# Kernel optimization log

Measured on AMD Instinct MI355X. Metric: run time of the kernel, lower is better.

The kernel has to match this reference:

```python
import jax, jax.numpy as jnp
import numpy as np

D_MODEL = 2048
D_STATE = 64
D_CONV = 4
EXPAND = 2
HEADDIM = 64
NGROUPS = 1
CHUNK = 64
D_INNER = D_MODEL * EXPAND          # 4096
NHEADS = D_INNER // HEADDIM         # 64
D_IN_PROJ = 2 * D_INNER + 2 * NGROUPS * D_STATE + NHEADS
BATCH, SEQLEN = 2, 4096
RMS_EPS = 1e-6


def elu_plus_one(x):
    return jax.nn.elu(x) + 1.0


def softplus(x):
    return jnp.where(x > 20, x, jnp.log1p(jnp.exp(x)))


def causal_conv1d(x, w, b):
    # x: (B, L, D), w: (K, D) depthwise kernel, b: (D,)
    Bsz, L, Dn = x.shape
    k = w.shape[0]
    xp = jnp.transpose(jnp.pad(x, ((0, 0), (k - 1, 0), (0, 0))), (0, 2, 1))  # (B, D, L+K-1)
    kern = jnp.transpose(w, (1, 0))[:, None, :]  # (D, 1, K)
    y = jax.lax.conv_general_dilated(xp, kern, (1,), 'VALID',
                                     feature_group_count=Dn,
                                     dimension_numbers=('NCH', 'OIH', 'NCH'))
    return jnp.transpose(y, (0, 2, 1)) + b


def ssd_chunked(q, k, v, a, chunk_size):
    # SSD / chunked linear attention with per-step scalar decay.
    # Recurrence: h_t = a_t * h_{t-1} + k_t v_t^T ; y_t = q_t @ h_t
    # q,k: (B,H,L,N); v: (B,H,L,P); a: (B,H,L) in (0,1)
    Bsz, H, L, N = q.shape
    S = chunk_size
    C = L // S
    qc = q.reshape(Bsz, H, C, S, N)
    kc = k.reshape(Bsz, H, C, S, N)
    vc = v.reshape(Bsz, H, C, S, -1)
    la = jnp.log(a).reshape(Bsz, H, C, S)
    cs = jnp.cumsum(la, axis=-1)                 # inclusive cumsum of log-decay within chunk
    causal = jnp.tril(jnp.ones((S, S), bool))
    # decay from position j to i (j<=i): exp(cs_i - cs_j)
    logdec = jnp.where(causal, cs[..., :, None] - cs[..., None, :], -jnp.inf)
    att = jnp.einsum('bhcsn,bhctn->bhcst', qc, kc) * jnp.exp(logdec)
    y_intra = jnp.einsum('bhcst,bhctp->bhcsp', att, vc)
    total = cs[..., -1]                           # (B,H,C) total log-decay per chunk
    k_scaled = kc * jnp.exp(total[..., None, None] - cs[..., None])
    states = jnp.einsum('bhcsn,bhcsp->bhcnp', k_scaled, vc)  # per-chunk state update
    d_t = jnp.moveaxis(jnp.exp(total), 2, 0)      # (C,B,H)
    s_t = jnp.moveaxis(states, 2, 0)              # (C,B,H,N,P)

    def step(h, inp):
        d, s = inp
        return d[..., None, None] * h + s, h      # emit state at chunk start

    _, h_prev = jax.lax.scan(step, jnp.zeros_like(s_t[0]), (d_t, s_t))
    h_prev = jnp.moveaxis(h_prev, 0, 2)           # (B,H,C,N,P)
    y_inter = jnp.einsum('bhcsn,bhcnp->bhcsp', qc * jnp.exp(cs)[..., None], h_prev)
    return (y_intra + y_inter).reshape(Bsz, H, L, -1)


def setup_inputs() -> dict:
    key = jax.random.key(0)
    k0, k1, k2, k3 = jax.random.split(key, 4)
    u = jax.random.normal(k0, (BATCH, SEQLEN, D_MODEL), jnp.float32)
    in_proj_w = jax.random.normal(k1, (D_MODEL, D_IN_PROJ), jnp.float32) / np.sqrt(D_MODEL)
    conv_weight = jax.random.normal(k2, (D_CONV, D_INNER), jnp.float32) / np.sqrt(D_CONV)
    conv_bias = jnp.zeros((D_INNER,), jnp.float32)
    A_log = jnp.log(jnp.linspace(1.0, 16.0, NHEADS)).astype(jnp.float32)
    dt_init = jnp.exp(jnp.linspace(np.log(0.001), np.log(0.1), NHEADS))
    dt_bias = (dt_init + jnp.log(-jnp.expm1(-dt_init))).astype(jnp.float32)
    D_param = jnp.ones((NHEADS,), jnp.float32)
    norm_scale = jnp.ones((D_INNER,), jnp.float32)
    out_proj_w = jax.random.normal(k3, (D_INNER, D_MODEL), jnp.float32) / np.sqrt(D_INNER)
    return dict(u=u, in_proj_w=in_proj_w, conv_weight=conv_weight, conv_bias=conv_bias,
                A_log=A_log, dt_bias=dt_bias, D_param=D_param, norm_scale=norm_scale,
                out_proj_w=out_proj_w)


def reference(u, in_proj_w, conv_weight, conv_bias, A_log, dt_bias, D_param, norm_scale, out_proj_w):
    Bsz, L, _ = u.shape
    zxBCdt = u @ in_proj_w
    splits = [D_INNER, 2 * D_INNER, 2 * D_INNER + NGROUPS * D_STATE, 2 * D_INNER + 2 * NGROUPS * D_STATE]
    z, x, B_proj, C_proj, dt_logits = jnp.split(zxBCdt, splits, axis=-1)
    x = jax.nn.silu(causal_conv1d(x, conv_weight, conv_bias))
    B_mat = elu_plus_one(B_proj.reshape(Bsz, L, NGROUPS, D_STATE))
    C_mat = elu_plus_one(C_proj.reshape(Bsz, L, NGROUPS, D_STATE))
    hpg = NHEADS // NGROUPS
    B_mat = jnp.repeat(B_mat, hpg, axis=2)   # (B,L,H,N)
    C_mat = jnp.repeat(C_mat, hpg, axis=2)
    dt = softplus(dt_logits + dt_bias)        # (B,L,H)
    a = jnp.exp(-dt * jnp.exp(A_log))         # (B,L,H), per-step decay
    x_heads = x.reshape(Bsz, L, NHEADS, HEADDIM)
    q = jnp.transpose(C_mat, (0, 2, 1, 3))
    k = jnp.transpose(B_mat, (0, 2, 1, 3))
    v = jnp.transpose(x_heads, (0, 2, 1, 3))
    a_t = jnp.transpose(a, (0, 2, 1))
    y = ssd_chunked(q, k, v, a_t, CHUNK)
    y = y + D_param[None, :, None, None] * v  # skip connection
    y = jnp.transpose(y, (0, 2, 1, 3)).reshape(Bsz, L, D_INNER)
    y = y * jax.lax.rsqrt(jnp.mean(y * y, axis=-1, keepdims=True) + RMS_EPS) * norm_scale
    y = y * jax.nn.silu(z)
    return y @ out_proj_w
```

## Files before the change

kernel.cpp:

```cpp
#include <hip/hip_runtime.h>
#include <hip/hip_bf16.h>
#include <cstdint>
#include <cstddef>

#define BATCH   2
#define SEQLEN  4096
#define DMODEL  2048
#define DINNER  4096
#define NHEADS  64
#define HEADDIM 64
#define DSTATE  64
#define CHUNK   64
#define NCHUNK  (SEQLEN/CHUNK)
#define DPROJ   8384
#define DPROJ_PAD 8448
#define MTOK    (BATCH*SEQLEN)
#define RMS_EPS 1e-6f

typedef __hip_bfloat16 bf16;
typedef __attribute__((ext_vector_type(8))) short bf16x8;
typedef __attribute__((ext_vector_type(4))) float f32x4;

__device__ __forceinline__ float siluf(float x) { return x / (1.f + expf(-x)); }
__device__ __forceinline__ float to_f(float x) { return x; }
__device__ __forceinline__ float to_f(bf16 x) { return __bfloat162float(x); }
__device__ __forceinline__ float bf2f(short s) { bf16 h; *(short*)&h = s; return __bfloat162float(h); }
__device__ __forceinline__ void from_f(float& d, float x) { d = x; }
__device__ __forceinline__ void from_f(bf16& d, float x) { d = __float2bfloat16(x); }

__device__ __forceinline__ void gload16(const void* g, void* l) {
  __builtin_amdgcn_global_load_lds(
      (const __attribute__((address_space(1))) void*)g,
      (__attribute__((address_space(3))) void*)l, 16, 0, 0);
}

template <typename TC, int KT>
__global__ __launch_bounds__(1024, 4) void gemm_w16p2(
    const bf16* __restrict__ A, int lda,
    const bf16* __restrict__ BT, int ldb,
    TC* __restrict__ C, int ldc, int gx) {
  __shared__ __align__(16) bf16 As[4 * 8192];
  __shared__ __align__(16) bf16 Bs[4 * 8192];
  const int tid  = threadIdx.x;
  const int lane = tid & 63;
  const int w    = tid >> 6;
  const int wm   = w >> 2;
  const int wn   = w & 3;
  const int lr   = lane & 15, lg = lane >> 4;
  const int fo   = 8 * (lg ^ ((lr >> 1) & 3));

  int nwg = gridDim.x;
  int bid = (int)blockIdx.x;
  int idx = (bid & 7) * (nwg >> 3) + (bid >> 3);
  int spos = idx % (8 * gx);
  const int m0 = ((idx / (8 * gx)) * 8 + (spos & 7)) * 256;
  const int n0 = (spos >> 3) * 256;

  const int srow = tid >> 2;
  const int ce   = 8 * ((tid & 3) ^ ((tid >> 3) & 3));
  const bf16* pA = A  + (size_t)(m0 + srow) * lda + ce;
  const bf16* pB = BT + (size_t)(n0 + srow) * ldb + ce;
  const int wofs = w * 512;
  const int aRd = (wm * 64 + lr) * 32 + fo;
  const int bRd = (wn * 64 + lr) * 32 + fo;

#define STAGE_A(kt) gload16(pA + ((kt) << 5), As + (((kt) & 3) << 13) + wofs)
#define STAGE_B(kt) gload16(pB + ((kt) << 5), Bs + (((kt) & 3) << 13) + wofs)

  f32x4 acc[4][4];
#pragma unroll
  for (int m = 0; m < 4; ++m)
#pragma unroll
    for (int n = 0; n < 4; ++n) acc[m][n] = (f32x4){0.f, 0.f, 0.f, 0.f};

#define TILE(T) do {                                                         \
    const bf16* Ab = As + (((T) & 3) << 13);                                 \
    const bf16* Bb = Bs + (((T) & 3) << 13);                                 \
    bf16x8 bfv[4], af[4];                                                    \
    _Pragma("unroll")                                                        \
    for (int n = 0; n < 4; ++n) bfv[n] = *(const bf16x8*)&Bb[bRd + n * 512]; \
    _Pragma("unroll")                                                        \
    for (int m = 0; m < 4; ++m) af[m] = *(const bf16x8*)&Ab[aRd + m * 512];  \
    asm volatile("s_waitcnt lgkmcnt(0)" ::: "memory");                       \
    __builtin_amdgcn_sched_barrier(0);                                       \
    __builtin_amdgcn_s_setprio(1);                                           \
    _Pragma("unroll")                                                        \
    for (int m = 0; m < 4; ++m)                                              \
      _Pragma("unroll")                                                      \
      for (int n = 0; n < 4; ++n)                                            \
        acc[m][n] = __builtin_amdgcn_mfma_f32_16x16x32_bf16(af[m], bfv[n], acc[m][n], 0, 0, 0); \
    __builtin_amdgcn_s_setprio(0);                                           \
  } while (0)

#define PERIOD(P, DOSTAGE) do {                                              \
    if (DOSTAGE) { STAGE_A(2 * (P) + 2); STAGE_B(2 * (P) + 2);               \
                   STAGE_A(2 * (P) + 3); STAGE_B(2 * (P) + 3); }             \
    TILE(2 * (P));                                                           \
    TILE(2 * (P) + 1);                                                       \
    asm volatile("s_waitcnt vmcnt(0)" ::: "memory");                         \
    __builtin_amdgcn_s_barrier();                                            \
    __builtin_amdgcn_sched_barrier(0);                                       \
  } while (0)

  STAGE_A(0); STAGE_B(0); STAGE_A(1); STAGE_B(1);
  asm volatile("s_waitcnt vmcnt(0)" ::: "memory");
  __builtin_amdgcn_s_barrier();
  __builtin_amdgcn_sched_barrier(0);

  const int NP = KT / 2;
#pragma unroll 2
  for (int p = 0; p < NP - 1; ++p) PERIOD(p, true);
  PERIOD(NP - 1, false);
#undef PERIOD
#undef TILE
#undef STAGE_A
#undef STAGE_B

  if constexpr (__is_same(TC, bf16)) {
    bf16* Ws = (w < 8 ? As : Bs) + (w & 7) * 4096;
#pragma unroll
    for (int m = 0; m < 4; ++m)
#pragma unroll
      for (int n = 0; n < 4; ++n)
#pragma unroll
        for (int reg = 0; reg < 4; ++reg) {
          int row = m * 16 + lg * 4 + reg;
          int slot = (n * 2 + (lr >> 3)) ^ (row & 7);
          Ws[row * 64 + slot * 8 + (lr & 7)] = __float2bfloat16(acc[m][n][reg]);
        }
    asm volatile("s_waitcnt lgkmcnt(0)" ::: "memory");
#pragma unroll
    for (int i = 0; i < 8; ++i) {
      int row = i * 8 + (lane >> 3);
      bf16x8 v = *(const bf16x8*)&Ws[row * 64 + ((lane & 7) ^ (lane >> 3)) * 8];
      int gcol = n0 + wn * 64 + (lane & 7) * 8;
      *(bf16x8*)&((bf16*)C)[(size_t)(m0 + wm * 64 + row) * ldc + gcol] = v;
    }
  } else {
#pragma unroll
    for (int m = 0; m < 4; ++m)
#pragma unroll
      for (int n = 0; n < 4; ++n) {
        int col = n0 + wn * 64 + n * 16 + lr;
        size_t rbase = (size_t)(m0 + wm * 64 + m * 16 + lg * 4);
#pragma unroll
        for (int reg = 0; reg < 4; ++reg)
          from_f(C[(rbase + reg) * ldc + col], acc[m][n][reg]);
      }
  }
}

template <typename TC, bool MASK>
__global__ __launch_bounds__(256) void gemm_mfma(
    const bf16* __restrict__ A, int lda,
    const bf16* __restrict__ BT, int ldb,
    TC* __restrict__ C, int ldc, int Kdim, int Nvalid) {
  __shared__ __align__(16) bf16 As[128 * 32];
  __shared__ __align__(16) bf16 Bs[128 * 32];
  const int tid  = threadIdx.x;
  const int lane = tid & 63;
  const int w    = tid >> 6;
  const int m0 = blockIdx.y * 128;
  const int n0 = blockIdx.x * 128;

  const int rs0 = w * 32 + (lane >> 2);
  const int ce  = 8 * ((lane & 3) ^ ((lane >> 2) & 3));
  const int fo  = 8 * ((lane >> 4) ^ (lane & 3));
  const int lr  = lane & 15, lg = lane >> 4;
  const int wr = w >> 1, wc = w & 1;

  f32x4 acc[4][4];
#pragma unroll
  for (int m = 0; m < 4; ++m)
#pragma unroll
    for (int n = 0; n < 4; ++n) acc[m][n] = (f32x4){0.f, 0.f, 0.f, 0.f};

  const size_t arow0 = (size_t)(m0 + rs0) * lda;
  const size_t arow1 = (size_t)(m0 + rs0 + 16) * lda;
  const size_t brow0 = (size_t)(n0 + rs0) * ldb;
  const size_t brow1 = (size_t)(n0 + rs0 + 16) * ldb;
  bf16* lA0 = &As[(w * 2 + 0) * 512];
  bf16* lA1 = &As[(w * 2 + 1) * 512];
  bf16* lB0 = &Bs[(w * 2 + 0) * 512];
  bf16* lB1 = &Bs[(w * 2 + 1) * 512];

  for (int k0 = 0; k0 < Kdim; k0 += 32) {
    __syncthreads();
    gload16(A + arow0 + k0 + ce, lA0);
    gload16(A + arow1 + k0 + ce, lA1);
    gload16(BT + brow0 + k0 + ce, lB0);
    gload16(BT + brow1 + k0 + ce, lB1);
    __syncthreads();
    bf16x8 af[4], bfr[4];
#pragma unroll
    for (int m = 0; m < 4; ++m)
      af[m] = *(const bf16x8*)&As[(wr * 64 + m * 16 + lr) * 32 + fo];
#pragma unroll
    for (int n = 0; n < 4; ++n)
      bfr[n] = *(const bf16x8*)&Bs[(wc * 64 + n * 16 + lr) * 32 + fo];
#pragma unroll
    for (int m = 0; m < 4; ++m)
#pragma unroll
      for (int n = 0; n < 4; ++n)
        acc[m][n] = __builtin_amdgcn_mfma_f32_16x16x32_bf16(af[m], bfr[n], acc[m][n], 0, 0, 0);
  }

#pragma unroll
  for (int m = 0; m < 4; ++m)
#pragma unroll
    for (int n = 0; n < 4; ++n) {
      int col = n0 + wc * 64 + n * 16 + lr;
      if (MASK && col >= Nvalid) continue;
      size_t rbase = (size_t)(m0 + wr * 64 + m * 16 + lg * 4);
#pragma unroll
      for (int reg = 0; reg < 4; ++reg)
        from_f(C[(rbase + reg) * ldc + col], acc[m][n][reg]);
    }
}

__global__ __launch_bounds__(256) void cast_bf16_kernel(
    const float* __restrict__ x, bf16* __restrict__ y) {
  size_t i = ((size_t)blockIdx.x * 256 + threadIdx.x) * 4;
  float4 v = *(const float4*)(x + i);
  y[i + 0] = __float2bfloat16(v.x);
  y[i + 1] = __float2bfloat16(v.y);
  y[i + 2] = __float2bfloat16(v.z);
  y[i + 3] = __float2bfloat16(v.w);
}

__global__ __launch_bounds__(256) void transpose_cast_kernel(
    const float* __restrict__ W, bf16* __restrict__ WT, int N, int K) {
  __shared__ float t[32][33];
  int n0 = blockIdx.x * 32, k0 = blockIdx.y * 32;
  int tx = threadIdx.x & 31, ty = threadIdx.x >> 5;
#pragma unroll
  for (int i = 0; i < 4; ++i) {
    int n = n0 + tx;
    t[ty + i * 8][tx] = (n < N) ? W[(size_t)(k0 + ty + i * 8) * N + n] : 0.f;
  }
  __syncthreads();
#pragma unroll
  for (int i = 0; i < 4; ++i) {
    int nn = ty + i * 8;
    WT[(size_t)(n0 + nn) * K + k0 + tx] = __float2bfloat16(t[tx][nn]);
  }
}

__global__ __launch_bounds__(256) void conv_silu_kernel(
    const bf16* __restrict__ zx, const float* __restrict__ cw,
    const float* __restrict__ cb, bf16* __restrict__ xc) {
  int idx = blockIdx.x * 256 + threadIdx.x;
  int d8 = (idx & 511) * 8;
  int g = idx >> 9;
  int m0 = g * 4;
  int l0 = m0 & (SEQLEN - 1);
  int b = m0 >> 12;
  bf16x8 rows[7];
  bf16x8 zvec;
#pragma unroll
  for (int j = 0; j < 8; ++j) zvec[j] = 0;
#pragma unroll
  for (int r = 0; r < 7; ++r) {
    int li = l0 - 3 + r;
    rows[r] = (li >= 0)
        ? *(const bf16x8*)&zx[(size_t)(b * SEQLEN + li) * DPROJ + DINNER + d8]
        : zvec;
  }
  float cwv[4][8], cbv[8];
#pragma unroll
  for (int k = 0; k < 4; ++k) {
    float4 a = *(const float4*)(cw + k * DINNER + d8);
    float4 bb = *(const float4*)(cw + k * DINNER + d8 + 4);
    cwv[k][0] = a.x; cwv[k][1] = a.y; cwv[k][2] = a.z; cwv[k][3] = a.w;
    cwv[k][4] = bb.x; cwv[k][5] = bb.y; cwv[k][6] = bb.z; cwv[k][7] = bb.w;
  }
  {
    float4 a = *(const float4*)(cb + d8);
    float4 bb = *(const float4*)(cb + d8 + 4);
    cbv[0] = a.x; cbv[1] = a.y; cbv[2] = a.z; cbv[3] = a.w;
    cbv[4] = bb.x; cbv[5] = bb.y; cbv[6] = bb.z; cbv[7] = bb.w;
  }
#pragma unroll
  for (int j = 0; j < 4; ++j) {
    float acc[8];
#pragma unroll
    for (int e = 0; e < 8; ++e) acc[e] = cbv[e];
#pragma unroll
    for (int k = 0; k < 4; ++k)
#pragma unroll
      for (int e = 0; e < 8; ++e) acc[e] += bf2f(rows[j + k][e]) * cwv[k][e];
    bf16x8 o;
#pragma unroll
    for (int e = 0; e < 8; ++e) { bf16 h = __float2bfloat16(siluf(acc[e])); o[e] = *(short*)&h; }
    *(bf16x8*)&xc[(size_t)(m0 + j) * DINNER + d8] = o;
  }
}

__global__ __launch_bounds__(256) void prep_cumsum_kernel(
    const bf16* __restrict__ zx, const float* __restrict__ A_log,
    const float* __restrict__ dt_bias, bf16* __restrict__ Bmb,
    bf16* __restrict__ Cmb, float* __restrict__ cs) {
  int bid = blockIdx.x;
  int c = bid & 63, b = bid >> 6;
  int m0 = b * SEQLEN + c * CHUNK;
  int tid = threadIdx.x;
  int s = tid >> 2, grp = (tid & 3) * 16;
  __shared__ float laT[64 * 65];
  __shared__ float segs[4][64];
  const bf16* row = zx + (size_t)(m0 + s) * DPROJ + 2 * DINNER;
  {
    union { bf16x8 v[2]; bf16 hh[16]; } u, o;
    u.v[0] = *(const bf16x8*)&row[grp];
    u.v[1] = *(const bf16x8*)&row[grp + 8];
#pragma unroll
    for (int i = 0; i < 16; ++i) {
      float bv = to_f(u.hh[i]);
      from_f(o.hh[i], bv > 0.f ? bv + 1.f : expf(bv));
    }
    *(bf16x8*)&Bmb[(size_t)(m0 + s) * 64 + grp] = o.v[0];
    *(bf16x8*)&Bmb[(size_t)(m0 + s) * 64 + grp + 8] = o.v[1];
    u.v[0] = *(const bf16x8*)&row[64 + grp];
    u.v[1] = *(const bf16x8*)&row[64 + grp + 8];
#pragma unroll
    for (int i = 0; i < 16; ++i) {
      float cv = to_f(u.hh[i]);
      from_f(o.hh[i], cv > 0.f ? cv + 1.f : expf(cv));
    }
    *(bf16x8*)&Cmb[(size_t)(m0 + s) * 64 + grp] = o.v[0];
    *(bf16x8*)&Cmb[(size_t)(m0 + s) * 64 + grp + 8] = o.v[1];
    u.v[0] = *(const bf16x8*)&row[128 + grp];
    u.v[1] = *(const bf16x8*)&row[128 + grp + 8];
#pragma unroll
    for (int i = 0; i < 16; ++i) {
      int j = grp + i;
      float dtl = to_f(u.hh[i]) + dt_bias[j];
      float dt = dtl > 20.f ? dtl : log1pf(expf(dtl));
      laT[j * 65 + s] = -dt * expf(A_log[j]);
    }
  }
  __syncthreads();
  int j = tid & 63, sg = tid >> 6;
  float p = 0.f;
#pragma unroll
  for (int i = 0; i < 16; ++i) p += laT[j * 65 + sg * 16 + i];
  segs[sg][j] = p;
  __syncthreads();
  float off = (sg > 0 ? segs[0][j] : 0.f) + (sg > 1 ? segs[1][j] : 0.f) +
              (sg > 2 ? segs[2][j] : 0.f);
  float acc = off;
#pragma unroll
  for (int i = 0; i < 16; ++i) {
    acc += laT[j * 65 + sg * 16 + i];
    cs[(size_t)(m0 + sg * 16 + i) * 64 + j] = acc;
  }
}

__global__ __launch_bounds__(256) void states_mfma(
    const bf16* __restrict__ Bmb, const bf16* __restrict__ xc,
    const float* __restrict__ cs, bf16* __restrict__ st) {
  int bid = blockIdx.x;
  int c = bid & 63, h = (bid >> 6) & 63, b = bid >> 12;
  int m0 = b * SEQLEN + c * CHUNK;
  int tid = threadIdx.x, lane = tid & 63, w = tid >> 6;
  int lr = lane & 15, lg = lane >> 4;
  __shared__ bf16 vT[64 * 72];
  __shared__ bf16 kT[64 * 72];
  int s4 = tid >> 2, c16 = (tid & 3) * 16;
  float cstot = cs[(size_t)(m0 + 63) * 64 + h];
  float ws = expf(cstot - cs[(size_t)(m0 + s4) * 64 + h]);
  {
    union { bf16x8 v[2]; bf16 hh[16]; } u;
    const bf16x8* pv = (const bf16x8*)&xc[(size_t)(m0 + s4) * DINNER + h * 64 + c16];
    u.v[0] = pv[0]; u.v[1] = pv[1];
#pragma unroll
    for (int i = 0; i < 16; ++i) vT[(c16 + i) * 72 + s4] = u.hh[i];
    const bf16x8* pk = (const bf16x8*)&Bmb[(size_t)(m0 + s4) * 64 + c16];
    u.v[0] = pk[0]; u.v[1] = pk[1];
#pragma unroll
    for (int i = 0; i < 16; ++i) kT[(c16 + i) * 72 + s4] = __float2bfloat16(to_f(u.hh[i]) * ws);
  }
  __syncthreads();
  f32x4 acc[4];
#pragma unroll
  for (int ct = 0; ct < 4; ++ct) acc[ct] = (f32x4){0.f, 0.f, 0.f, 0.f};
#pragma unroll
  for (int ks = 0; ks < 2; ++ks) {
    bf16x8 af = *(const bf16x8*)&vT[(w * 16 + lr) * 72 + ks * 32 + lg * 8];
#pragma unroll
    for (int ct = 0; ct < 4; ++ct) {
      bf16x8 bf_ = *(const bf16x8*)&kT[(ct * 16 + lr) * 72 + ks * 32 + lg * 8];
      acc[ct] = __builtin_amdgcn_mfma_f32_16x16x32_bf16(af, bf_, acc[ct], 0, 0, 0);
    }
  }
  size_t ob = (((size_t)(b * NHEADS + h)) * NCHUNK + c) * 4096;
#pragma unroll
  for (int ct = 0; ct < 4; ++ct) {
    int n = ct * 16 + lr;
#pragma unroll
    for (int r = 0; r < 4; ++r) {
      int p = w * 16 + lg * 4 + r;
      from_f(st[ob + (size_t)p * 64 + n], acc[ct][r]);
    }
  }
}

__global__ __launch_bounds__(256) void scan_kernel(
    const float* __restrict__ cs, bf16* __restrict__ st) {
  int bid = blockIdx.x;
  int bh = bid >> 2, qq = bid & 3;
  int b = bh >> 6, h = bh & 63;
  int tid = threadIdx.x;
  __shared__ float dec[64];
  if (tid < 64)
    dec[tid] = expf(cs[(size_t)(b * SEQLEN + tid * CHUNK + 63) * 64 + h]);
  int e0 = qq * 1024 + tid * 4;
  float hr[4] = {0.f, 0.f, 0.f, 0.f};
  size_t base = (size_t)bh * NCHUNK * 4096;
  typedef __attribute__((ext_vector_type(4))) short bf16x4;
  union U { bf16x4 v; bf16 hh[4]; };
  U buf[4];
  buf[0].v = *(bf16x4*)(st + base + 0 * 4096 + e0);
  buf[1].v = *(bf16x4*)(st + base + 1 * 4096 + e0);
  buf[2].v = *(bf16x4*)(st + base + 2 * 4096 + e0);
  __syncthreads();
#pragma unroll 4
  for (int c = 0; c < NCHUNK; ++c) {
    if (c + 3 < NCHUNK)
      buf[(c + 3) & 3].v = *(bf16x4*)(st + base + (size_t)(c + 3) * 4096 + e0);
    float d = dec[c];
    U out;
#pragma unroll
    for (int i = 0; i < 4; ++i) {
      float sv = to_f(buf[c & 3].hh[i]);
      from_f(out.hh[i], hr[i]);
      hr[i] = d * hr[i] + sv;
    }
    *(bf16x4*)(st + base + (size_t)c * 4096 + e0) = out.v;
  }
}

__global__ __launch_bounds__(256) void chunk_out_mfma(
    const bf16* __restrict__ Bmb, const bf16* __restrict__ Cmb,
    const bf16* __restrict__ xc, const float* __restrict__ cs,
    const bf16* __restrict__ st, const float* __restrict__ Dp,
    bf16* __restrict__ zx) {
  int bid = blockIdx.x;
  int c = bid & 63, h = (bid >> 6) & 63, b = bid >> 12;
  int m0 = b * SEQLEN + c * CHUNK;
  int tid = threadIdx.x, lane = tid & 63, w = tid >> 6;
  int lr = lane & 15, lg = lane >> 4;
  __shared__ bf16 qL[64 * 72];
  __shared__ bf16 kL[64 * 72];
  __shared__ bf16 A2[64 * 136];
  __shared__ bf16 B2[64 * 136];
  __shared__ float csl[64];
  int s4 = tid >> 2, c16 = (tid & 3) * 16;

  if (tid < 64) csl[tid] = cs[(size_t)(m0 + tid) * 64 + h];
  {
    const bf16x8* pq = (const bf16x8*)&Cmb[(size_t)(m0 + s4) * 64 + c16];
    *(bf16x8*)&qL[s4 * 72 + c16] = pq[0];
    *(bf16x8*)&qL[s4 * 72 + c16 + 8] = pq[1];
    const bf16x8* pk = (const bf16x8*)&Bmb[(size_t)(m0 + s4) * 64 + c16];
    *(bf16x8*)&kL[s4 * 72 + c16] = pk[0];
    *(bf16x8*)&kL[s4 * 72 + c16 + 8] = pk[1];
  }
  {
    union { bf16x8 v[2]; bf16 hh[16]; } u;
    const bf16x8* pv = (const bf16x8*)&xc[(size_t)(m0 + s4) * DINNER + h * 64 + c16];
    u.v[0] = pv[0]; u.v[1] = pv[1];
#pragma unroll
    for (int i = 0; i < 16; ++i) B2[(c16 + i) * 136 + s4] = u.hh[i];
  }
  {
    size_t hb = (((size_t)(b * NHEADS + h)) * NCHUNK + c) * 4096;
    const bf16x8* ph = (const bf16x8*)&st[hb + (size_t)s4 * 64 + c16];
    *(bf16x8*)&B2[s4 * 136 + 64 + c16] = ph[0];
    *(bf16x8*)&B2[s4 * 136 + 64 + c16 + 8] = ph[1];
  }
  __syncthreads();

  f32x4 acc1[4];
#pragma unroll
  for (int ct = 0; ct < 4; ++ct) acc1[ct] = (f32x4){0.f, 0.f, 0.f, 0.f};
#pragma unroll
  for (int ks = 0; ks < 2; ++ks) {
    bf16x8 af = *(const bf16x8*)&qL[(w * 16 + lr) * 72 + ks * 32 + lg * 8];
#pragma unroll
    for (int ct = 0; ct < 4; ++ct) {
      bf16x8 bf_ = *(const bf16x8*)&kL[(ct * 16 + lr) * 72 + ks * 32 + lg * 8];
      acc1[ct] = __builtin_amdgcn_mfma_f32_16x16x32_bf16(af, bf_, acc1[ct], 0, 0, 0);
    }
  }
  {
    float es = expf(csl[s4]);
    union { bf16x8 v[2]; bf16 hh[16]; } u;
    const bf16x8* pq = (const bf16x8*)&qL[s4 * 72 + c16];
    u.v[0] = pq[0]; u.v[1] = pq[1];
#pragma unroll
    for (int i = 0; i < 16; ++i) u.hh[i] = __float2bfloat16(to_f(u.hh[i]) * es);
    *(bf16x8*)&A2[s4 * 136 + 64 + c16] = u.v[0];
    *(bf16x8*)&A2[s4 * 136 + 64 + c16 + 8] = u.v[1];
  }
#pragma unroll
  for (int ct = 0; ct < 4; ++ct) {
    int t = ct * 16 + lr;
#pragma unroll
    for (int r = 0; r < 4; ++r) {
      int s = w * 16 + lg * 4 + r;
      float val = (t <= s) ? acc1[ct][r] * expf(csl[s] - csl[t]) : 0.f;
      A2[s * 136 + t] = __float2bfloat16(val);
    }
  }
  __syncthreads();

  float Dh = Dp[h];
  f32x4 acc2[4];
#pragma unroll
  for (int ct = 0; ct < 4; ++ct) {
    int p = ct * 16 + lr;
#pragma unroll
    for (int r = 0; r < 4; ++r)
      acc2[ct][r] = Dh * to_f(B2[p * 136 + (w * 16 + lg * 4 + r)]);
  }
#pragma unroll
  for (int ks = 0; ks < 4; ++ks) {
    bf16x8 af = *(const bf16x8*)&A2[(w * 16 + lr) * 136 + ks * 32 + lg * 8];
#pragma unroll
    for (int ct = 0; ct < 4; ++ct) {
      bf16x8 bf_ = *(const bf16x8*)&B2[(ct * 16 + lr) * 136 + ks * 32 + lg * 8];
      acc2[ct] = __builtin_amdgcn_mfma_f32_16x16x32_bf16(af, bf_, acc2[ct], 0, 0, 0);
    }
  }
  __syncthreads();
#pragma unroll
  for (int ct = 0; ct < 4; ++ct) {
    int p = ct * 16 + lr;
#pragma unroll
    for (int r = 0; r < 4; ++r)
      qL[(w * 16 + lg * 4 + r) * 72 + p] = __float2bfloat16(acc2[ct][r]);
  }
  __syncthreads();
  {
    const bf16x8* py = (const bf16x8*)&qL[s4 * 72 + c16];
    bf16x8* pg = (bf16x8*)&zx[(size_t)(m0 + s4) * DPROJ + DINNER + h * 64 + c16];
    pg[0] = py[0]; pg[1] = py[1];
  }
}

__global__ __launch_bounds__(256) void rmsnorm_gate_kernel(
    bf16* __restrict__ zx, const float* __restrict__ scale) {
  int m = blockIdx.x;
  int tid = threadIdx.x;
  bf16* row = zx + (size_t)m * DPROJ;
  float vals[16];
  float ss = 0.f;
#pragma unroll
  for (int g = 0; g < 2; ++g) {
    int d8 = (tid + g * 256) * 8;
    bf16x8 yv = *(const bf16x8*)&row[DINNER + d8];
#pragma unroll
    for (int j = 0; j < 8; ++j) {
      float y = bf2f(yv[j]);
      vals[g * 8 + j] = y;
      ss += y * y;
    }
  }
#pragma unroll
  for (int off = 32; off > 0; off >>= 1) ss += __shfl_down(ss, off, 64);
  __shared__ float red[4];
  if ((tid & 63) == 0) red[tid >> 6] = ss;
  __syncthreads();
  float tot = red[0] + red[1] + red[2] + red[3];
  float inv = rsqrtf(tot / (float)DINNER + RMS_EPS);
#pragma unroll
  for (int g = 0; g < 2; ++g) {
    int d8 = (tid + g * 256) * 8;
    bf16x8 zv = *(const bf16x8*)&row[d8];
    const float* sc = scale + d8;
    bf16x8 o;
#pragma unroll
    for (int j = 0; j < 8; ++j) {
      bf16 hh = __float2bfloat16(vals[g * 8 + j] * inv * sc[j] * siluf(bf2f(zv[j])));
      o[j] = *(short*)&hh;
    }
    *(bf16x8*)&row[DINNER + d8] = o;
  }
}

extern "C" void kernel_launch(void* const* d_in, const int* in_sizes, int n_in,
                              void* d_out, int out_size, void* d_ws, size_t ws_size,
                              hipStream_t stream) {
  const float* u       = (const float*)d_in[0];
  const float* Win     = (const float*)d_in[1];
  const float* cw      = (const float*)d_in[2];
  const float* cb      = (const float*)d_in[3];
  const float* A_log   = (const float*)d_in[4];
  const float* dt_bias = (const float*)d_in[5];
  const float* Dp      = (const float*)d_in[6];
  const float* nscale  = (const float*)d_in[7];
  const float* Wout    = (const float*)d_in[8];
  float* out = (float*)d_out;

  bf16* zx = (bf16*)d_ws;
  bf16* xc = zx + (size_t)MTOK * DPROJ;
  bf16* ub = xc;
  bf16* wT = xc + (size_t)MTOK * DINNER;
  bf16* Bmb = wT + (size_t)DPROJ_PAD * DMODEL;
  bf16* Cmb = Bmb + (size_t)MTOK * 64;
  float* cs = (float*)(Cmb + (size_t)MTOK * 64);
  bf16* st = (bf16*)d_out;

  cast_bf16_kernel<<<(MTOK * DMODEL) / (256 * 4), 256, 0, stream>>>(u, ub);
  transpose_cast_kernel<<<dim3(DPROJ_PAD / 32, DMODEL / 32), 256, 0, stream>>>(Win, wT, DPROJ, DMODEL);
  gemm_w16p2<bf16, DMODEL / 32><<<(2 * DINNER / 256) * (MTOK / 256), 1024, 0, stream>>>(
      ub, DMODEL, wT, DMODEL, zx, DPROJ, 2 * DINNER / 256);
  gemm_mfma<bf16, true><<<dim3(2, MTOK / 128), 256, 0, stream>>>(
      ub, DMODEL, wT + (size_t)(2 * DINNER) * DMODEL, DMODEL,
      zx + 2 * DINNER, DPROJ, DMODEL, 192);
  transpose_cast_kernel<<<dim3(DMODEL / 32, DINNER / 32), 256, 0, stream>>>(Wout, wT, DMODEL, DINNER);
  conv_silu_kernel<<<(MTOK / 4) * 512 / 256, 256, 0, stream>>>(zx, cw, cb, xc);
  prep_cumsum_kernel<<<BATCH * NCHUNK, 256, 0, stream>>>(zx, A_log, dt_bias, Bmb, Cmb, cs);
  states_mfma<<<BATCH * NHEADS * NCHUNK, 256, 0, stream>>>(Bmb, xc, cs, st);
  scan_kernel<<<BATCH * NHEADS * 4, 256, 0, stream>>>(cs, st);
  chunk_out_mfma<<<BATCH * NHEADS * NCHUNK, 256, 0, stream>>>(Bmb, Cmb, xc, cs, st, Dp, zx);
  rmsnorm_gate_kernel<<<MTOK, 256, 0, stream>>>(zx, nscale);
  gemm_w16p2<float, DINNER / 32><<<(DMODEL / 256) * (MTOK / 256), 1024, 0, stream>>>(
      zx + DINNER, DPROJ, wT, DINNER, out, DMODEL, DMODEL / 256);
}
```

Before: 635.4 us.

## Add 4-stage pipelined in-proj GEMM and smaller-tile B/C/dt GEMM

Adds a new gemm_w16 kernel with a four-buffer LDS pipeline that prefetches three K-tiles ahead, uses explicit vmcnt waits and raw s_barrier, and raises wave priority around the MFMA block. It replaces gemm_w16p2 for the large input projection. The narrow B/C/dt projection GEMM is also rewritten to 32-row M tiles with 128-thread blocks, giving many more workgroups for the small-N tail. The explicit waitcnt choreography risks subtle ordering bugs and relies on exact per-thread load counts.

```diff
diff --git a/kernel.cpp b/kernel.cpp
--- a/kernel.cpp
+++ b/kernel.cpp
@@ -32,6 +32,116 @@
   __builtin_amdgcn_global_load_lds(
       (const __attribute__((address_space(1))) void*)g,
       (__attribute__((address_space(3))) void*)l, 16, 0, 0);
+}
+
+template <typename TC, int KT>
+__global__ __launch_bounds__(1024, 4) void gemm_w16(
+    const bf16* __restrict__ A, int lda,
+    const bf16* __restrict__ BT, int ldb,
+    TC* __restrict__ C, int ldc, int gx) {
+  __shared__ __align__(16) bf16 As[4 * 8192];
+  __shared__ __align__(16) bf16 Bs[4 * 8192];
+  const int tid  = threadIdx.x;
+  const int lane = tid & 63;
+  const int w    = tid >> 6;
+  const int wm   = w >> 2;
+  const int wn   = w & 3;
+  const int lr   = lane & 15, lg = lane >> 4;
+  const int fo   = 8 * (lg ^ ((lr >> 1) & 3));
+
+  int nwg = gridDim.x;
+  int bid = (int)blockIdx.x;
+  int idx = (bid & 7) * (nwg >> 3) + (bid >> 3);
+  int spos = idx % (8 * gx);
+  const int m0 = ((idx / (8 * gx)) * 8 + (spos & 7)) * 256;
+  const int n0 = (spos >> 3) * 256;
+
+  const int srow = tid >> 2;
+  const int ce   = 8 * ((tid & 3) ^ ((tid >> 3) & 3));
+  const bf16* pA = A  + (size_t)(m0 + srow) * lda + ce;
+  const bf16* pB = BT + (size_t)(n0 + srow) * ldb + ce;
+  const int wofs = w * 512;
+  const int aRd = (wm * 64 + lr) * 32 + fo;
+  const int bRd = (wn * 64 + lr) * 32 + fo;
+
+#define STAGE_A(kt) gload16(pA + ((kt) << 5), As + (((kt) & 3) << 13) + wofs)
+#define STAGE_B(kt) gload16(pB + ((kt) << 5), Bs + (((kt) & 3) << 13) + wofs)
+
+  f32x4 acc[4][4];
+#pragma unroll
+  for (int m = 0; m < 4; ++m)
+#pragma unroll
+    for (int n = 0; n < 4; ++n) acc[m][n] = (f32x4){0.f, 0.f, 0.f, 0.f};
+
+#define KBODY(T, DOSTAGE, VMC) do {                                          \
+    const bf16* Ab = As + (((T) & 3) << 13);                                 \
+    const bf16* Bb = Bs + (((T) & 3) << 13);                                 \
+    if (DOSTAGE) { STAGE_A((T) + 3); STAGE_B((T) + 3); }                     \
+    bf16x8 bfv[4], af[4];                                                    \
+    _Pragma("unroll")                                                        \
+    for (int n = 0; n < 4; ++n) bfv[n] = *(const bf16x8*)&Bb[bRd + n * 512]; \
+    _Pragma("unroll")                                                        \
+    for (int m = 0; m < 4; ++m) af[m] = *(const bf16x8*)&Ab[aRd + m * 512];  \
+    asm volatile("s_waitcnt lgkmcnt(0)" ::: "memory");                       \
+    __builtin_amdgcn_sched_barrier(0);                                       \
+    __builtin_amdgcn_s_setprio(1);                                           \
+    _Pragma("unroll")                                                        \
+    for (int m = 0; m < 4; ++m)                                              \
+      _Pragma("unroll")                                                      \
+      for (int n = 0; n < 4; ++n)                                            \
+        acc[m][n] = __builtin_amdgcn_mfma_f32_16x16x32_bf16(af[m], bfv[n], acc[m][n], 0, 0, 0); \
+    __builtin_amdgcn_s_setprio(0);                                           \
+    asm volatile("s_waitcnt vmcnt(" #VMC ")" ::: "memory");                  \
+    __builtin_amdgcn_s_barrier();                                            \
+    __builtin_amdgcn_sched_barrier(0);                                       \
+  } while (0)
+
+  STAGE_A(0); STAGE_B(0); STAGE_A(1); STAGE_B(1); STAGE_A(2); STAGE_B(2);
+  asm volatile("s_waitcnt vmcnt(4)" ::: "memory");
+  __builtin_amdgcn_s_barrier();
+  __builtin_amdgcn_sched_barrier(0);
+
+#pragma unroll 4
+  for (int t = 0; t < KT - 3; ++t) KBODY(t, true, 4);
+  KBODY(KT - 3, false, 2);
+  KBODY(KT - 2, false, 0);
+  KBODY(KT - 1, false, 0);
+#undef KBODY
+#undef STAGE_A
+#undef STAGE_B
+
+  if constexpr (__is_same(TC, bf16)) {
+    bf16* Ws = (w < 8 ? As : Bs) + (w & 7) * 4096;
+#pragma unroll
+    for (int m = 0; m < 4; ++m)
+#pragma unroll
+      for (int n = 0; n < 4; ++n)
+#pragma unroll
+        for (int reg = 0; reg < 4; ++reg) {
+          int row = m * 16 + lg * 4 + reg;
+          int slot = (n * 2 + (lr >> 3)) ^ (row & 7);
+          Ws[row * 64 + slot * 8 + (lr & 7)] = __float2bfloat16(acc[m][n][reg]);
+        }
+    asm volatile("s_waitcnt lgkmcnt(0)" ::: "memory");
+#pragma unroll
+    for (int i = 0; i < 8; ++i) {
+      int row = i * 8 + (lane >> 3);
+      bf16x8 v = *(const bf16x8*)&Ws[row * 64 + ((lane & 7) ^ (lane >> 3)) * 8];
+      int gcol = n0 + wn * 64 + (lane & 7) * 8;
+      *(bf16x8*)&((bf16*)C)[(size_t)(m0 + wm * 64 + row) * ldc + gcol] = v;
+    }
+  } else {
+#pragma unroll
+    for (int m = 0; m < 4; ++m)
+#pragma unroll
+      for (int n = 0; n < 4; ++n) {
+        int col = n0 + wn * 64 + n * 16 + lr;
+        size_t rbase = (size_t)(m0 + wm * 64 + m * 16 + lg * 4);
+#pragma unroll
+        for (int reg = 0; reg < 4; ++reg)
+          from_f(C[(rbase + reg) * ldc + col], acc[m][n][reg]);
+      }
+  }
 }
 
 template <typename TC, int KT>
@@ -150,68 +260,62 @@
   }
 }
 
-template <typename TC, bool MASK>
-__global__ __launch_bounds__(256) void gemm_mfma(
+template <typename TC>
+__global__ __launch_bounds__(128) void gemm_bcdt(
     const bf16* __restrict__ A, int lda,
     const bf16* __restrict__ BT, int ldb,
     TC* __restrict__ C, int ldc, int Kdim, int Nvalid) {
-  __shared__ __align__(16) bf16 As[128 * 32];
+  __shared__ __align__(16) bf16 As[32 * 32];
   __shared__ __align__(16) bf16 Bs[128 * 32];
   const int tid  = threadIdx.x;
   const int lane = tid & 63;
   const int w    = tid >> 6;
-  const int m0 = blockIdx.y * 128;
+  const int lr   = lane & 15, lg = lane >> 4;
+  const int fo   = 8 * (lg ^ (lr & 3));
+  const int m0 = blockIdx.y * 32;
   const int n0 = blockIdx.x * 128;
 
-  const int rs0 = w * 32 + (lane >> 2);
-  const int ce  = 8 * ((lane & 3) ^ ((lane >> 2) & 3));
-  const int fo  = 8 * ((lane >> 4) ^ (lane & 3));
-  const int lr  = lane & 15, lg = lane >> 4;
-  const int wr = w >> 1, wc = w & 1;
-
-  f32x4 acc[4][4];
-#pragma unroll
-  for (int m = 0; m < 4; ++m)
+  const int srow = tid >> 2;
+  const int ce   = 8 * ((tid & 3) ^ ((tid >> 2) & 3));
+  const bf16* pA = A  + (size_t)(m0 + srow) * lda + ce;
+  const bf16* pB = BT + (size_t)(n0 + srow) * ldb + ce;
+  const int dof = w * 512;
+
+  f32x4 acc[2][4];
+#pragma unroll
+  for (int m = 0; m < 2; ++m)
 #pragma unroll
     for (int n = 0; n < 4; ++n) acc[m][n] = (f32x4){0.f, 0.f, 0.f, 0.f};
-
-  const size_t arow0 = (size_t)(m0 + rs0) * lda;
-  const size_t arow1 = (size_t)(m0 + rs0 + 16) * lda;
-  const size_t brow0 = (size_t)(n0 + rs0) * ldb;
-  const size_t brow1 = (size_t)(n0 + rs0 + 16) * ldb;
-  bf16* lA0 = &As[(w * 2 + 0) * 512];
-  bf16* lA1 = &As[(w * 2 + 1) * 512];
-  bf16* lB0 = &Bs[(w * 2 + 0) * 512];
-  bf16* lB1 = &Bs[(w * 2 + 1) * 512];
 
   for (int k0 = 0; k0 < Kdim; k0 += 32) {
     __syncthreads();
-    gload16(A + arow0 + k0 + ce, lA0);
-    gload16(A + arow1 + k0 + ce, lA1);
-    gload16(BT + brow0 + k0 + ce, lB0);
-    gload16(BT + brow1 + k0 + ce, lB1);
+    gload16(pA + k0, As + dof);
+    gload16(pB + k0,                   Bs + 0 * 1024 + dof);
+    gload16(pB + (size_t)32 * ldb + k0, Bs + 1 * 1024 + dof);
+    gload16(pB + (size_t)64 * ldb + k0, Bs + 2 * 1024 + dof);
+    gload16(pB + (size_t)96 * ldb + k0, Bs + 3 * 1024 + dof);
     __syncthreads();
-    bf16x8 af[4], bfr[4];
-#pragma unroll
-    for (int m = 0; m < 4; ++m)
-      af[m] = *(const bf16x8*)&As[(wr * 64 + m * 16 + lr) * 32 + fo];
+    bf16x8 af[2], bfr[4];
+#pragma unroll
+    for (int m = 0; m < 2; ++m)
+      af[m] = *(const bf16x8*)&As[(m * 16 + lr) * 32 + fo];
 #pragma unroll
     for (int n = 0; n < 4; ++n)
-      bfr[n] = *(const bf16x8*)&Bs[(wc * 64 + n * 16 + lr) * 32 + fo];
-#pragma unroll
-    for (int m = 0; m < 4; ++m)
+      bfr[n] = *(const bf16x8*)&Bs[(w * 64 + n * 16 + lr) * 32 + fo];
+#pragma unroll
+    for (int m = 0; m < 2; ++m)
 #pragma unroll
       for (int n = 0; n < 4; ++n)
         acc[m][n] = __builtin_amdgcn_mfma_f32_16x16x32_bf16(af[m], bfr[n], acc[m][n], 0, 0, 0);
   }
 
 #pragma unroll
-  for (int m = 0; m < 4; ++m)
+  for (int m = 0; m < 2; ++m)
 #pragma unroll
     for (int n = 0; n < 4; ++n) {
-      int col = n0 + wc * 64 + n * 16 + lr;
-      if (MASK && col >= Nvalid) continue;
-      size_t rbase = (size_t)(m0 + wr * 64 + m * 16 + lg * 4);
+      int col = n0 + w * 64 + n * 16 + lr;
+      if (col >= Nvalid) continue;
+      size_t rbase = (size_t)(m0 + m * 16 + lg * 4);
 #pragma unroll
       for (int reg = 0; reg < 4; ++reg)
         from_f(C[(rbase + reg) * ldc + col], acc[m][n][reg]);
@@ -613,9 +717,9 @@
 
   cast_bf16_kernel<<<(MTOK * DMODEL) / (256 * 4), 256, 0, stream>>>(u, ub);
   transpose_cast_kernel<<<dim3(DPROJ_PAD / 32, DMODEL / 32), 256, 0, stream>>>(Win, wT, DPROJ, DMODEL);
-  gemm_w16p2<bf16, DMODEL / 32><<<(2 * DINNER / 256) * (MTOK / 256), 1024, 0, stream>>>(
+  gemm_w16<bf16, DMODEL / 32><<<(2 * DINNER / 256) * (MTOK / 256), 1024, 0, stream>>>(
       ub, DMODEL, wT, DMODEL, zx, DPROJ, 2 * DINNER / 256);
-  gemm_mfma<bf16, true><<<dim3(2, MTOK / 128), 256, 0, stream>>>(
+  gemm_bcdt<bf16><<<dim3(2, MTOK / 32), 128, 0, stream>>>(
       ub, DMODEL, wT + (size_t)(2 * DINNER) * DMODEL, DMODEL,
       zx + 2 * DINNER, DPROJ, DMODEL, 192);
   transpose_cast_kernel<<<dim3(DMODEL / 32, DINNER / 32), 256, 0, stream>>>(Wout, wT, DMODEL, DINNER);
```

Measured after the change: 635.2 us. No clear change (-0.0%).
